# Performance work log

Measured on AMD Instinct MI355X. Metric: run time of the kernel, lower is better.

The kernel has to match this reference:

```python
import jax, jax.numpy as jnp
import numpy as np

TEMP = 0.5
EPS = 1e-8  # torch CosineSimilarity eps


def setup_inputs() -> dict:
    key = jax.random.key(0)
    k1, k2 = jax.random.split(key)
    B, D = 4096, 256
    return {
        "features1": jax.random.normal(k1, (B, D), dtype=jnp.float32),
        "features2": jax.random.normal(k2, (B, D), dtype=jnp.float32),
    }


def reference(features1, features2):
    B = features1.shape[0]
    f = jnp.concatenate([features1, features2], axis=0)  # [2B, D]
    # cosine similarity matrix via norms + GEMM (same math as broadcasted cos)
    n = jnp.sqrt(jnp.sum(f * f, axis=-1))  # [2B]
    dots = f @ f.T  # [2B, 2B]
    logits = dots / jnp.maximum(n[:, None] * n[None, :], EPS) / TEMP
    # labels = cat([arange(B), arange(B)]) -- faithful to the source module
    labels = jnp.concatenate([jnp.arange(B), jnp.arange(B)], axis=0)  # [2B]
    lse = jax.nn.logsumexp(logits, axis=1)  # [2B]
    picked = logits[jnp.arange(2 * B), labels]  # [2B]
    return jnp.mean(lse - picked)
```

## Files before the change

### kernel.cpp

```cpp
#include <hip/hip_runtime.h>
#include <hip/hip_bf16.h>
#include <math.h>


#define B_ROWS 4096
#define D_DIM  256
#define N_ROWS 8192
#define NPANEL 64

typedef __attribute__((ext_vector_type(8))) short short8;
typedef __attribute__((ext_vector_type(4))) float f32x4;

__global__ __launch_bounds__(256) void nt_norm_picked(
    const float* __restrict__ f1, const float* __restrict__ f2,
    unsigned short* __restrict__ G, float* __restrict__ picked_cross,
    float* __restrict__ prow) {
  __shared__ float4 vbuf[2][64];
  __shared__ float ssbuf[2];
  const int tid = threadIdx.x, lane = tid & 63, w = tid >> 6;
  const int zidx = blockIdx.x * 256 + tid;
  if (zidx < 32768) reinterpret_cast<float4*>(prow)[zidx] = float4{0.f, 0.f, 0.f, 0.f};
  const int pl = w >> 1, src = w & 1;
  const int p = blockIdx.x * 2 + pl;
  const float* rowp = (src == 0 ? f1 : f2) + (size_t)p * D_DIM;
  float4 v = reinterpret_cast<const float4*>(rowp)[lane];
  float ss = v.x * v.x + v.y * v.y + v.z * v.z + v.w * v.w;
#pragma unroll
  for (int m = 1; m < 64; m <<= 1) ss += __shfl_xor(ss, m, 64);
  const float scale = 1.41421356237309515f * rsqrtf(fmaxf(ss, 1e-30f));
  union { ushort4 u; __hip_bfloat16 h[4]; } pk;
  pk.h[0] = __float2bfloat16(v.x * scale);
  pk.h[1] = __float2bfloat16(v.y * scale);
  pk.h[2] = __float2bfloat16(v.z * scale);
  pk.h[3] = __float2bfloat16(v.w * scale);
  const int grow = p + src * B_ROWS;
  reinterpret_cast<ushort4*>(G + (size_t)grow * D_DIM)[lane] = pk.u;
  if (src == 0) { vbuf[pl][lane] = v; if (lane == 0) ssbuf[pl] = ss; }
  __syncthreads();
  if (src == 1) {
    float4 u = vbuf[pl][lane];
    float d = v.x * u.x + v.y * u.y + v.z * u.z + v.w * u.w;
#pragma unroll
    for (int m = 1; m < 64; m <<= 1) d += __shfl_xor(d, m, 64);
    if (lane == 0)
      picked_cross[p] = 2.0f * d * rsqrtf(ss) * rsqrtf(ssbuf[pl]);
  }
}

__device__ __forceinline__ void stage_lds(const char* gsrc_base, char* lds_base,
                                          int tid) {
  const int lane = tid & 63, wid = tid >> 6;
#pragma unroll
  for (int r = 0; r < 8; ++r) {
    const int o  = r * 4096 + wid * 1024 + lane * 16;
    const int so = o ^ (((o >> 9) & 7) << 4);
    __builtin_amdgcn_global_load_lds(
        (const __attribute__((address_space(1))) void*)(gsrc_base + so),
        (__attribute__((address_space(3))) void*)(lds_base + r * 4096 + wid * 1024),
        16, 0, 0);
  }
}

__global__ __launch_bounds__(256, 2) void nt_gemm_tri(
    const unsigned short* __restrict__ G,
    float* __restrict__ prow,
    float* __restrict__ pcol)
{
  const int bid = blockIdx.x;
  const int p   = bid & 31;
  const int k   = bid >> 5;
  const int rbA = 63 - p;
  const int n1  = 2 * (rbA + 1);
  const int t0  = (130 * k) >> 4;
  const int t1  = (130 * (k + 1)) >> 4;

  const int tid = threadIdx.x, lane = tid & 63, wid = tid >> 6;
  const int l15 = lane & 15, q16 = (lane >> 4) << 4;

  __shared__ short8 lds8[4096];
  char* ldsb = reinterpret_cast<char*>(lds8);
  const char* gb = reinterpret_cast<const char*>(G);

  short8 af[2][8];
  int rb = (t0 < n1) ? rbA : p;
  {
    const int sb0 = (t0 < n1) ? t0 : t0 - n1;
    stage_lds(gb + (size_t)sb0 * 32768, ldsb, tid);
  }
#pragma unroll
  for (int m = 0; m < 2; ++m) {
    const size_t ro = (size_t)(rb * 128 + wid * 32 + m * 16 + l15) * 512;
#pragma unroll
    for (int ks = 0; ks < 8; ++ks)
      af[m][ks] = *reinterpret_cast<const short8*>(gb + ro + ks * 64 + q16);
  }
  float rs[8];
#pragma unroll
  for (int i = 0; i < 8; ++i) rs[i] = 0.f;
  __syncthreads();

  for (int t = t0; t < t1; ++t) {
    char* bbuf = ldsb + ((t - t0) & 1) * 32768;
    if (t + 1 < t1) {
      const int sbn = (t + 1 < n1) ? t + 1 : t + 1 - n1;
      stage_lds(gb + (size_t)sbn * 32768, ldsb + ((t + 1 - t0) & 1) * 32768, tid);
    }
    const int sb = (t < n1) ? t : t - n1;

    f32x4 acc[2][4] = {};
#pragma unroll
    for (int ks = 0; ks < 8; ++ks) {
      short8 bf[4];
#pragma unroll
      for (int n = 0; n < 4; ++n) {
        const int brow = n * 16 + l15;
        const int off  = (brow * 512 + ks * 64 + q16) ^ ((brow & 7) << 4);
        bf[n] = *reinterpret_cast<const short8*>(bbuf + off);
      }
#pragma unroll
      for (int m = 0; m < 2; ++m)
#pragma unroll
        for (int n = 0; n < 4; ++n)
          acc[m][n] = __builtin_amdgcn_mfma_f32_16x16x32_bf16(
              af[m][ks], bf[n], acc[m][n], 0, 0, 0);
    }

    float cs[4] = {0.f, 0.f, 0.f, 0.f};
#pragma unroll
    for (int m = 0; m < 2; ++m)
#pragma unroll
      for (int n = 0; n < 4; ++n)
#pragma unroll
        for (int j = 0; j < 4; ++j) {
          const float e = __expf(acc[m][n][j]);
          rs[m * 4 + j] += e;
          cs[n] += e;
        }
    if ((sb >> 1) != rb) {
#pragma unroll
      for (int n = 0; n < 4; ++n) {
        float c = cs[n];
        c += __shfl_xor(c, 16, 64);
        c += __shfl_xor(c, 32, 64);
        if (lane < 16)
          pcol[(size_t)(4 * rb + wid) * N_ROWS + sb * 64 + n * 16 + lane] = c;
      }
    }

    const bool last = (t + 1 == t1);
    const bool swi  = (t + 1 == n1) && !last;
    if (last || swi) {
#pragma unroll
      for (int i = 0; i < 8; ++i) {
        float v = rs[i];
        v += __shfl_xor(v, 1, 64);
        v += __shfl_xor(v, 2, 64);
        v += __shfl_xor(v, 4, 64);
        v += __shfl_xor(v, 8, 64);
        rs[i] = v;
      }
      if (l15 == 0) {
        const int g = lane >> 4;
#pragma unroll
        for (int i = 0; i < 8; ++i)
          prow[(size_t)k * N_ROWS + rb * 128 + wid * 32 + (i >> 2) * 16 + g * 4 + (i & 3)] = rs[i];
      }
#pragma unroll
      for (int i = 0; i < 8; ++i) rs[i] = 0.f;
    }
    if (swi) {
      rb = p;
#pragma unroll
      for (int m = 0; m < 2; ++m) {
        const size_t ro = (size_t)(rb * 128 + wid * 32 + m * 16 + l15) * 512;
#pragma unroll
        for (int ks = 0; ks < 8; ++ks)
          af[m][ks] = *reinterpret_cast<const short8*>(gb + ro + ks * 64 + q16);
      }
    }
    __syncthreads();
  }
}

__global__ __launch_bounds__(128) void nt_finalize1(
    const float* __restrict__ prow, const float* __restrict__ pcol,
    const float* __restrict__ picked_cross, float* __restrict__ loss_part) {
  const int q = blockIdx.x, tid = threadIdx.x;
  const int r = q * 128 + tid;
  float s = 0.f;
#pragma unroll
  for (int j = 0; j < 16; ++j) s += prow[(size_t)j * N_ROWS + r];
  for (int rb = q + 1; rb < NPANEL; ++rb) {
    const float* b = pcol + (size_t)(4 * rb) * N_ROWS + r;
    s += b[0] + b[(size_t)N_ROWS] + b[(size_t)2 * N_ROWS] + b[(size_t)3 * N_ROWS];
  }
  const float pick = (r < B_ROWS) ? 2.0f : picked_cross[r - B_ROWS];
  float local = __logf(s) - pick;
#pragma unroll
  for (int m = 1; m < 64; m <<= 1) local += __shfl_xor(local, m, 64);
  __shared__ float red[2];
  if ((tid & 63) == 0) red[tid >> 6] = local;
  __syncthreads();
  if (tid == 0) loss_part[q] = red[0] + red[1];
}

__global__ __launch_bounds__(64) void nt_finalize2(
    const float* __restrict__ loss_part, float* __restrict__ out) {
  const int tid = threadIdx.x;
  float v = loss_part[tid];
#pragma unroll
  for (int m = 1; m < 64; m <<= 1) v += __shfl_xor(v, m, 64);
  if (tid == 0) out[0] = v / (float)N_ROWS;
}

extern "C" void kernel_launch(void* const* d_in, const int* in_sizes, int n_in,
                              void* d_out, int out_size, void* d_ws, size_t ws_size,
                              hipStream_t stream) {
  const float* f1 = (const float*)d_in[0];
  const float* f2 = (const float*)d_in[1];
  float* out = (float*)d_out;

  char* ws = (char*)d_ws;
  unsigned short* G   = (unsigned short*)ws;
  float* prow         = (float*)(ws + (size_t)4 * 1024 * 1024);
  float* pcol         = (float*)(ws + (size_t)5 * 1024 * 1024);
  float* picked_cross = (float*)(ws + (size_t)13 * 1024 * 1024);
  float* loss_part    = (float*)(ws + (size_t)13 * 1024 * 1024 + 64 * 1024);

  hipLaunchKernelGGL(nt_norm_picked, dim3(B_ROWS / 2), dim3(256), 0, stream,
                     f1, f2, G, picked_cross, prow);
  hipLaunchKernelGGL(nt_gemm_tri, dim3(512), dim3(256), 0, stream,
                     G, prow, pcol);
  hipLaunchKernelGGL(nt_finalize1, dim3(NPANEL), dim3(128), 0, stream,
                     prow, pcol, picked_cross, loss_part);
  hipLaunchKernelGGL(nt_finalize2, dim3(1), dim3(64), 0, stream,
                     loss_part, out);
}
```

Before: 59.89 us.

## Retile GEMM waves to 2x2 layout with atomic row sums, parallelize finalize

Each wave of the triangular GEMM now covers a 64x32 sub-tile (2x2 wave grid) instead of 32x64. This halves the LDS B-fragment reads per wave but doubles the A fragments held in registers. Two waves now share each output row, so row partial sums are combined with atomicAdd into prow, and column partials are stored at half the row granularity, shrinking pcol. The finalize kernel is split across 128 blocks, with one wave reading prow and three waves striding over pcol panels. The cost is higher register pressure and atomic traffic.

```diff
diff --git a/kernel.cpp b/kernel.cpp
--- a/kernel.cpp
+++ b/kernel.cpp
@@ -75,75 +75,74 @@
   const int t1  = (130 * (k + 1)) >> 4;
 
   const int tid = threadIdx.x, lane = tid & 63, wid = tid >> 6;
+  const int wr = wid >> 1, wc = wid & 1;
   const int l15 = lane & 15, q16 = (lane >> 4) << 4;
 
   __shared__ short8 lds8[4096];
   char* ldsb = reinterpret_cast<char*>(lds8);
   const char* gb = reinterpret_cast<const char*>(G);
 
-  short8 af[2][8];
   int rb = (t0 < n1) ? rbA : p;
-  {
-    const int sb0 = (t0 < n1) ? t0 : t0 - n1;
-    stage_lds(gb + (size_t)sb0 * 32768, ldsb, tid);
-  }
-#pragma unroll
-  for (int m = 0; m < 2; ++m) {
-    const size_t ro = (size_t)(rb * 128 + wid * 32 + m * 16 + l15) * 512;
-#pragma unroll
-    for (int ks = 0; ks < 8; ++ks)
+  stage_lds(gb + (t0 < n1 ? t0 : t0 - n1) * 32768, ldsb, tid);
+
+  short8 af[4][8];
+#pragma unroll
+  for (int m = 0; m < 4; ++m) {
+    const int ro = (rb * 128 + wr * 64 + m * 16 + l15) * 512;
+#pragma unroll
+    for (int ks = 0; ks < 8; ++ks) {
       af[m][ks] = *reinterpret_cast<const short8*>(gb + ro + ks * 64 + q16);
-  }
-  float rs[8];
-#pragma unroll
-  for (int i = 0; i < 8; ++i) rs[i] = 0.f;
+      asm volatile("" : "+v"(af[m][ks]));
+    }
+  }
+  float rs[16];
+#pragma unroll
+  for (int i = 0; i < 16; ++i) rs[i] = 0.f;
   __syncthreads();
 
   for (int t = t0; t < t1; ++t) {
     char* bbuf = ldsb + ((t - t0) & 1) * 32768;
     if (t + 1 < t1) {
       const int sbn = (t + 1 < n1) ? t + 1 : t + 1 - n1;
-      stage_lds(gb + (size_t)sbn * 32768, ldsb + ((t + 1 - t0) & 1) * 32768, tid);
+      stage_lds(gb + sbn * 32768, ldsb + ((t + 1 - t0) & 1) * 32768, tid);
     }
     const int sb = (t < n1) ? t : t - n1;
 
-    f32x4 acc[2][4] = {};
+    f32x4 acc[4][2] = {};
 #pragma unroll
     for (int ks = 0; ks < 8; ++ks) {
-      short8 bf[4];
-#pragma unroll
-      for (int n = 0; n < 4; ++n) {
-        const int brow = n * 16 + l15;
+      short8 bf[2];
+#pragma unroll
+      for (int n = 0; n < 2; ++n) {
+        const int brow = wc * 32 + n * 16 + l15;
         const int off  = (brow * 512 + ks * 64 + q16) ^ ((brow & 7) << 4);
         bf[n] = *reinterpret_cast<const short8*>(bbuf + off);
       }
 #pragma unroll
-      for (int m = 0; m < 2; ++m)
-#pragma unroll
-        for (int n = 0; n < 4; ++n)
+      for (int m = 0; m < 4; ++m)
+#pragma unroll
+        for (int n = 0; n < 2; ++n)
           acc[m][n] = __builtin_amdgcn_mfma_f32_16x16x32_bf16(
               af[m][ks], bf[n], acc[m][n], 0, 0, 0);
     }
 
-    float cs[4] = {0.f, 0.f, 0.f, 0.f};
-#pragma unroll
-    for (int m = 0; m < 2; ++m)
-#pragma unroll
-      for (int n = 0; n < 4; ++n)
-#pragma unroll
-        for (int j = 0; j < 4; ++j) {
-          const float e = __expf(acc[m][n][j]);
-          rs[m * 4 + j] += e;
-          cs[n] += e;
-        }
+    float cs0 = 0.f, cs1 = 0.f;
+#pragma unroll
+    for (int m = 0; m < 4; ++m)
+#pragma unroll
+      for (int j = 0; j < 4; ++j) {
+        const float e0 = __expf(acc[m][0][j]);
+        const float e1 = __expf(acc[m][1][j]);
+        rs[m * 4 + j] += e0 + e1;
+        cs0 += e0; cs1 += e1;
+      }
     if ((sb >> 1) != rb) {
-#pragma unroll
-      for (int n = 0; n < 4; ++n) {
-        float c = cs[n];
-        c += __shfl_xor(c, 16, 64);
-        c += __shfl_xor(c, 32, 64);
-        if (lane < 16)
-          pcol[(size_t)(4 * rb + wid) * N_ROWS + sb * 64 + n * 16 + lane] = c;
+      cs0 += __shfl_xor(cs0, 16, 64); cs0 += __shfl_xor(cs0, 32, 64);
+      cs1 += __shfl_xor(cs1, 16, 64); cs1 += __shfl_xor(cs1, 32, 64);
+      if (lane < 16) {
+        float* dst = pcol + (size_t)(2 * rb + wr) * N_ROWS + sb * 64 + wc * 32 + lane;
+        dst[0]  = cs0;
+        dst[16] = cs1;
       }
     }
 
@@ -151,7 +150,7 @@
     const bool swi  = (t + 1 == n1) && !last;
     if (last || swi) {
 #pragma unroll
-      for (int i = 0; i < 8; ++i) {
+      for (int i = 0; i < 16; ++i) {
         float v = rs[i];
         v += __shfl_xor(v, 1, 64);
         v += __shfl_xor(v, 2, 64);
@@ -162,55 +161,70 @@
       if (l15 == 0) {
         const int g = lane >> 4;
 #pragma unroll
-        for (int i = 0; i < 8; ++i)
-          prow[(size_t)k * N_ROWS + rb * 128 + wid * 32 + (i >> 2) * 16 + g * 4 + (i & 3)] = rs[i];
-      }
-#pragma unroll
-      for (int i = 0; i < 8; ++i) rs[i] = 0.f;
+        for (int i = 0; i < 16; ++i)
+          atomicAdd(&prow[(size_t)k * N_ROWS + rb * 128 + wr * 64 +
+                          (i >> 2) * 16 + g * 4 + (i & 3)], rs[i]);
+      }
+#pragma unroll
+      for (int i = 0; i < 16; ++i) rs[i] = 0.f;
     }
     if (swi) {
       rb = p;
 #pragma unroll
-      for (int m = 0; m < 2; ++m) {
-        const size_t ro = (size_t)(rb * 128 + wid * 32 + m * 16 + l15) * 512;
-#pragma unroll
-        for (int ks = 0; ks < 8; ++ks)
+      for (int m = 0; m < 4; ++m) {
+        const int ro = (rb * 128 + wr * 64 + m * 16 + l15) * 512;
+#pragma unroll
+        for (int ks = 0; ks < 8; ++ks) {
           af[m][ks] = *reinterpret_cast<const short8*>(gb + ro + ks * 64 + q16);
+          asm volatile("" : "+v"(af[m][ks]));
+        }
       }
     }
     __syncthreads();
   }
 }
 
-__global__ __launch_bounds__(128) void nt_finalize1(
+__global__ __launch_bounds__(256) void nt_finalize1(
     const float* __restrict__ prow, const float* __restrict__ pcol,
     const float* __restrict__ picked_cross, float* __restrict__ loss_part) {
-  const int q = blockIdx.x, tid = threadIdx.x;
-  const int r = q * 128 + tid;
+  const int blk = blockIdx.x, tid = threadIdx.x;
+  const int pan = blk >> 1;
+  const int l   = tid & 63;
+  const int r   = pan * 128 + (blk & 1) * 64 + l;
+  const int g   = tid >> 6;
   float s = 0.f;
-#pragma unroll
-  for (int j = 0; j < 16; ++j) s += prow[(size_t)j * N_ROWS + r];
-  for (int rb = q + 1; rb < NPANEL; ++rb) {
-    const float* b = pcol + (size_t)(4 * rb) * N_ROWS + r;
-    s += b[0] + b[(size_t)N_ROWS] + b[(size_t)2 * N_ROWS] + b[(size_t)3 * N_ROWS];
-  }
-  const float pick = (r < B_ROWS) ? 2.0f : picked_cross[r - B_ROWS];
-  float local = __logf(s) - pick;
-#pragma unroll
-  for (int m = 1; m < 64; m <<= 1) local += __shfl_xor(local, m, 64);
-  __shared__ float red[2];
-  if ((tid & 63) == 0) red[tid >> 6] = local;
-  __syncthreads();
-  if (tid == 0) loss_part[q] = red[0] + red[1];
-}
-
-__global__ __launch_bounds__(64) void nt_finalize2(
+  if (g == 0) {
+#pragma unroll
+    for (int j = 0; j < 16; ++j) s += prow[(size_t)j * N_ROWS + r];
+  } else {
+    for (int rb = pan + g; rb < NPANEL; rb += 3) {
+      s += pcol[(size_t)(2 * rb) * N_ROWS + r];
+      s += pcol[(size_t)(2 * rb + 1) * N_ROWS + r];
+    }
+  }
+  __shared__ float red[4][64];
+  red[g][l] = s;
+  __syncthreads();
+  if (g == 0) {
+    float tot = red[0][l] + red[1][l] + red[2][l] + red[3][l];
+    const float pick = (r < B_ROWS) ? 2.0f : picked_cross[r - B_ROWS];
+    float local = __logf(tot) - pick;
+#pragma unroll
+    for (int m = 1; m < 64; m <<= 1) local += __shfl_xor(local, m, 64);
+    if (l == 0) loss_part[blk] = local;
+  }
+}
+
+__global__ __launch_bounds__(128) void nt_finalize2(
     const float* __restrict__ loss_part, float* __restrict__ out) {
   const int tid = threadIdx.x;
   float v = loss_part[tid];
 #pragma unroll
   for (int m = 1; m < 64; m <<= 1) v += __shfl_xor(v, m, 64);
-  if (tid == 0) out[0] = v / (float)N_ROWS;
+  __shared__ float red[2];
+  if ((tid & 63) == 0) red[tid >> 6] = v;
+  __syncthreads();
+  if (tid == 0) out[0] = (red[0] + red[1]) / (float)N_ROWS;
 }
 
 extern "C" void kernel_launch(void* const* d_in, const int* in_sizes, int n_in,
@@ -224,15 +238,15 @@
   unsigned short* G   = (unsigned short*)ws;
   float* prow         = (float*)(ws + (size_t)4 * 1024 * 1024);
   float* pcol         = (float*)(ws + (size_t)5 * 1024 * 1024);
-  float* picked_cross = (float*)(ws + (size_t)13 * 1024 * 1024);
-  float* loss_part    = (float*)(ws + (size_t)13 * 1024 * 1024 + 64 * 1024);
+  float* picked_cross = (float*)(ws + (size_t)9 * 1024 * 1024);
+  float* loss_part    = (float*)(ws + (size_t)9 * 1024 * 1024 + 64 * 1024);
 
   hipLaunchKernelGGL(nt_norm_picked, dim3(B_ROWS / 2), dim3(256), 0, stream,
                      f1, f2, G, picked_cross, prow);
   hipLaunchKernelGGL(nt_gemm_tri, dim3(512), dim3(256), 0, stream,
                      G, prow, pcol);
-  hipLaunchKernelGGL(nt_finalize1, dim3(NPANEL), dim3(128), 0, stream,
+  hipLaunchKernelGGL(nt_finalize1, dim3(128), dim3(256), 0, stream,
                      prow, pcol, picked_cross, loss_part);
-  hipLaunchKernelGGL(nt_finalize2, dim3(1), dim3(64), 0, stream,
+  hipLaunchKernelGGL(nt_finalize2, dim3(1), dim3(128), 0, stream,
                      loss_part, out);
 }
```

Result: no change. 58.80 us (-1.8%).
